# Kernel optimization log

Measured on AMD Instinct MI355X. Metric: run time of the kernel, lower is better.

The kernel has to match this reference:

```python
import jax, jax.numpy as jnp
import numpy as np

B, S, D = 2, 2048, 768
H, STRIDE = 12, 8
HD = D // H  # 64


def setup_inputs() -> dict:
    key = jax.random.key(0)
    k0, k1, k2 = jax.random.split(key, 3)
    x = jax.random.normal(k0, (B, S, D), dtype=jnp.float32)
    qkv_w = jax.random.normal(k1, (3 * D, D), dtype=jnp.float32) * 0.02
    qkv_b = jnp.zeros((3 * D,), dtype=jnp.float32)
    out_w = jax.random.normal(k2, (D, D), dtype=jnp.float32) * 0.02
    out_b = jnp.zeros((D,), dtype=jnp.float32)
    return {"x": x, "qkv_w": qkv_w, "qkv_b": qkv_b, "out_w": out_w, "out_b": out_b}


def _stride_mask(S, stride, causal):
    i = jnp.arange(S)[:, None]
    j = jnp.arange(S)[None, :]
    strided = (j % stride == 0)
    if causal:
        strided = strided & (j <= i)
    # diagonal always attended; previous token attended for i > 0
    return strided | (j == i) | (j == i - 1)


def reference(x, qkv_w, qkv_b, out_w, out_b):
    Bx, Sx, Dx = x.shape
    qkv = x @ qkv_w.T + qkv_b                      # [B,S,3D]
    qkv = qkv.reshape(Bx, Sx, 3, H, HD)
    q, k, v = jnp.transpose(qkv, (2, 0, 3, 1, 4))  # each [B,H,S,HD]
    scale = HD ** -0.5
    attn = jnp.einsum('bhid,bhjd->bhij', q, k) * scale  # [B,H,S,S]
    mask = _stride_mask(Sx, STRIDE, True)          # [S,S] bool
    attn = jnp.where(mask[None, None], attn, -jnp.inf)
    a = jax.nn.softmax(attn, axis=-1)
    # every row has at least the diagonal unmasked, so no NaN rows;
    # nan_to_num kept for exact parity with the torch module
    a = jnp.nan_to_num(a, nan=0.0)
    out = jnp.einsum('bhij,bhjd->bhid', a, v)      # [B,H,S,HD]
    out = jnp.transpose(out, (0, 2, 1, 3)).reshape(Bx, Sx, Dx)
    return out @ out_w.T + out_b
```

## Files before the change

### kernel.cpp

```cpp
#include <hip/hip_runtime.h>
#include <hip/hip_bf16.h>
#include <stdint.h>

#define H_   12
#define S_   2048
#define D_   768
#define HD_  64
#define MS_  256

typedef __bf16 bf16_8 __attribute__((ext_vector_type(8)));
typedef float  f32_4  __attribute__((ext_vector_type(4)));

typedef __attribute__((address_space(1))) void* gas_ptr;
typedef __attribute__((address_space(3))) void* las_ptr;

__device__ __forceinline__ void g2l16(const void* g, void* l) {
  __builtin_amdgcn_global_load_lds((gas_ptr)g, (las_ptr)l, 16, 0, 0);
}

__device__ __forceinline__ f32_4 mfma16(bf16_8 a, bf16_8 b, f32_4 c) {
  return __builtin_amdgcn_mfma_f32_16x16x32_bf16(a, b, c, 0, 0, 0);
}

__device__ __forceinline__ bf16_8 ld8(const __hip_bfloat16* p) {
  return *reinterpret_cast<const bf16_8*>(p);
}

__global__ __launch_bounds__(256) void cvt3_f32_bf16(
    const float* __restrict__ a, const float* __restrict__ b,
    const float* __restrict__ c, __hip_bfloat16* __restrict__ out,
    int na4, int nb4) {
  const int t = blockIdx.x * 256 + threadIdx.x;
  float4 f;
  if (t < na4)            f = reinterpret_cast<const float4*>(a)[t];
  else if (t < na4 + nb4) f = reinterpret_cast<const float4*>(b)[t - na4];
  else                    f = reinterpret_cast<const float4*>(c)[t - na4 - nb4];
  union { __hip_bfloat16 h[4]; ushort4 u; } p;
  p.h[0] = __float2bfloat16(f.x);
  p.h[1] = __float2bfloat16(f.y);
  p.h[2] = __float2bfloat16(f.z);
  p.h[3] = __float2bfloat16(f.w);
  reinterpret_cast<ushort4*>(out)[t] = p.u;
}

template <int MODE, int BN>
__global__ __launch_bounds__(256, 2) void gemm_bt(
    const __hip_bfloat16* __restrict__ A, const __hip_bfloat16* __restrict__ B,
    const float* __restrict__ bias,
    __hip_bfloat16* __restrict__ O0, __hip_bfloat16* __restrict__ O1,
    __hip_bfloat16* __restrict__ O2, __hip_bfloat16* __restrict__ O3,
    __hip_bfloat16* __restrict__ O4, float* __restrict__ OF,
    int M, int N, int K) {
  constexpr int NTJ = BN / 32;
  __shared__ __bf16 sA[128 * 32];
  __shared__ __bf16 sB[BN * 32];
  const int tid  = threadIdx.x;
  const int lane = tid & 63;
  const int wv   = tid >> 6;
  const int m0 = blockIdx.y * 128;
  const int n0 = blockIdx.x * BN;
  const int wr = (wv >> 1) * 64;
  const int wc = (wv & 1) * (BN / 2);

  f32_4 acc[4][NTJ] = {};

  const __hip_bfloat16* aS = A + (size_t)(m0 + (tid >> 2)) * K + ((tid & 3) << 3);
  const __hip_bfloat16* bS = B + (size_t)(n0 + (tid >> 2)) * K + ((tid & 3) << 3);
  const size_t half = (size_t)64 * K;
  __bf16* dA  = &sA[tid * 8];
  __bf16* dA2 = &sA[tid * 8 + 2048];
  __bf16* dB  = &sB[tid * 8];
  __bf16* dB2 = &sB[tid * 8 + 2048];

  const int fr = lane & 15;
  const int kq = (lane >> 4) << 3;

  for (int k0 = 0; k0 < K; k0 += 32) {
    g2l16(aS, dA);
    g2l16(aS + half, dA2);
    g2l16(bS, dB);
    if constexpr (BN == 128) g2l16(bS + half, dB2);
    aS += 32;
    bS += 32;
    __syncthreads();
    bf16_8 af[4], bfm[NTJ];
#pragma unroll
    for (int t = 0; t < 4; ++t)
      af[t] = *reinterpret_cast<const bf16_8*>(&sA[(wr + t * 16 + fr) * 32 + kq]);
#pragma unroll
    for (int t = 0; t < NTJ; ++t)
      bfm[t] = *reinterpret_cast<const bf16_8*>(&sB[(wc + t * 16 + fr) * 32 + kq]);
#pragma unroll
    for (int ti = 0; ti < 4; ++ti)
#pragma unroll
      for (int tj = 0; tj < NTJ; ++tj)
        acc[ti][tj] = mfma16(af[ti], bfm[tj], acc[ti][tj]);
    __syncthreads();
  }

  const int crow = (lane >> 4) << 2;
  const int ccol = lane & 15;
#pragma unroll
  for (int ti = 0; ti < 4; ++ti) {
    const int gmb = m0 + wr + ti * 16 + crow;
#pragma unroll
    for (int tj = 0; tj < NTJ; ++tj) {
      const int gn = n0 + wc + tj * 16 + ccol;
      const float bv = bias[gn];
      if (MODE == 0) {
        const int t   = gn / D_;
        const int rem = gn - t * D_;
        const int hh = rem >> 6, dd = rem & 63;
        __hip_bfloat16* dst = (t == 0) ? O0 : (t == 1) ? O1 : O2;
#pragma unroll
        for (int r = 0; r < 4; ++r) {
          const int gm = gmb + r;
          const int bb = gm >> 11, ss = gm & (S_ - 1);
          const __hip_bfloat16 hv = __float2bfloat16(acc[ti][tj][r] + bv);
          dst[(((size_t)(bb * H_ + hh) << 11) + ss) * HD_ + dd] = hv;
          if (r == 0 && (gmb & 7) == 0) {
            if (t == 1)
              O4[(((size_t)(bb * H_ + hh)) * MS_ + (ss >> 3)) * HD_ + dd] = hv;
            else if (t == 2)
              O3[((size_t)(bb * H_ + hh) * HD_ + dd) * MS_ + (ss >> 3)] = hv;
          }
        }
      } else {
#pragma unroll
        for (int r = 0; r < 4; ++r)
          OF[(size_t)(gmb + r) * D_ + gn] = acc[ti][tj][r] + bv;
      }
    }
  }
}

__global__ __launch_bounds__(256) void attn_mfma(
    const __hip_bfloat16* __restrict__ Q, const __hip_bfloat16* __restrict__ Kb,
    const __hip_bfloat16* __restrict__ Ks, const __hip_bfloat16* __restrict__ Vr,
    const __hip_bfloat16* __restrict__ VsT, __hip_bfloat16* __restrict__ ctx) {
  __shared__ __bf16 pt[4][16 * 40];
  __shared__ float ox[2][64][20];
  const int lane = threadIdx.x & 63;
  const int wv   = threadIdx.x >> 6;
  const int tp   = wv >> 1;
  const int part = wv & 1;
  const int task = blockIdx.x * 2 + tp;
  const int bh   = task >> 7;
  const int i0   = (task & 127) << 4;
  const int lr   = lane & 15;
  const int quad = lane >> 4;
  const float SC = 0.125f * 1.44269504088896340736f;

  const __hip_bfloat16* Kh  = Kb  + ((size_t)bh << 11) * HD_;
  const __hip_bfloat16* Ksh = Ks  + (size_t)bh * MS_ * HD_;
  const __hip_bfloat16* Vrh = Vr  + ((size_t)bh << 11) * HD_;
  const __hip_bfloat16* Vsh = VsT + (size_t)bh * HD_ * MS_;
  __bf16* ptw = pt[wv];

  const int jbase = (i0 >= 8) ? (i0 - 8) : 0;

  bf16_8 vfb[4], kb_[2][2];
  if (part) {
    const __bf16* Vrb = reinterpret_cast<const __bf16*>(Vrh);
#pragma unroll
    for (int ct = 0; ct < 4; ++ct)
#pragma unroll
      for (int e = 0; e < 8; ++e) {
        const int j  = jbase + quad * 8 + e;
        const int jr = (j < S_) ? j : (S_ - 1);
        vfb[ct][e] = Vrb[(size_t)jr * HD_ + ct * 16 + lr];
      }
#pragma unroll
    for (int t = 0; t < 2; ++t) {
      const int j  = jbase + t * 16 + lr;
      const int jr = (j < S_) ? j : (S_ - 1);
      const __hip_bfloat16* kp = Kh + (size_t)jr * HD_ + quad * 8;
      kb_[t][0] = ld8(kp);
      kb_[t][1] = ld8(kp + 32);
    }
  }

  const __hip_bfloat16* qp = Q + (((size_t)bh << 11) + i0 + lr) * HD_ + quad * 8;
  const bf16_8 qf0 = ld8(qp);
  const bf16_8 qf1 = ld8(qp + 32);

  const __bf16 one = (__bf16)1.0f;
  const bf16_8 onesf = {one, one, one, one, one, one, one, one};

  f32_4 Lacc = {}, oacc[4];
#pragma unroll
  for (int ct = 0; ct < 4; ++ct) oacc[ct] = f32_4{0.f, 0.f, 0.f, 0.f};

  const int mmax = (i0 + 15) >> 3;
  const int nstr = (mmax >> 5) + 1;

  auto load_str = [&](int c, bf16_8 (&kf)[2][2], bf16_8 (&vf)[4]) {
    const int mb = c << 5;
#pragma unroll
    for (int t = 0; t < 2; ++t) {
      const __hip_bfloat16* kp = Ksh + (size_t)(mb + t * 16 + lr) * HD_ + quad * 8;
      kf[t][0] = ld8(kp);
      kf[t][1] = ld8(kp + 32);
    }
#pragma unroll
    for (int ct = 0; ct < 4; ++ct)
      vf[ct] = ld8(Vsh + (size_t)(ct * 16 + lr) * MS_ + mb + quad * 8);
  };

  auto softmax_pv = [&](f32_4& s0, f32_4& s1, const bf16_8 (&vf)[4]) {
#pragma unroll
    for (int r = 0; r < 4; ++r) {
      const int row = quad * 4 + r;
      ptw[row * 40 + lr]      = (__bf16)__float2bfloat16(s0[r]);
      ptw[row * 40 + 16 + lr] = (__bf16)__float2bfloat16(s1[r]);
    }
    const bf16_8 pf = *reinterpret_cast<const bf16_8*>(&ptw[lr * 40 + quad * 8]);
#pragma unroll
    for (int ct = 0; ct < 4; ++ct) oacc[ct] = mfma16(pf, vf[ct], oacc[ct]);
    Lacc = mfma16(pf, onesf, Lacc);
  };

  bf16_8 kf[2][2], vf[4], kf2[2][2], vf2[4];
  if (part < nstr) load_str(part, kf, vf);
  for (int c = part; c < nstr; c += 2) {
    const bool more = (c + 2 < nstr);
    if (more) load_str(c + 2, kf2, vf2);
    const int mb = c << 5;

    f32_4 s0 = {}, s1 = {};
    s0 = mfma16(qf0, kf[0][0], s0);
    s0 = mfma16(qf1, kf[0][1], s0);
    s1 = mfma16(qf0, kf[1][0], s1);
    s1 = mfma16(qf1, kf[1][1], s1);

#pragma unroll
    for (int r = 0; r < 4; ++r) {
      const int i = i0 + quad * 4 + r;
      const bool v0 = ((mb + lr) << 3) <= i;
      const bool v1 = ((mb + 16 + lr) << 3) <= i;
      s0[r] = v0 ? exp2f(fminf(s0[r] * SC, 63.f)) : 0.f;
      s1[r] = v1 ? exp2f(fminf(s1[r] * SC, 63.f)) : 0.f;
    }
    softmax_pv(s0, s1, vf);

    if (more) {
#pragma unroll
      for (int t = 0; t < 2; ++t) { kf[t][0] = kf2[t][0]; kf[t][1] = kf2[t][1]; }
#pragma unroll
      for (int ct = 0; ct < 4; ++ct) vf[ct] = vf2[ct];
    }
  }

  if (part) {
    f32_4 s0 = {}, s1 = {};
    s0 = mfma16(qf0, kb_[0][0], s0);
    s0 = mfma16(qf1, kb_[0][1], s0);
    s1 = mfma16(qf0, kb_[1][0], s1);
    s1 = mfma16(qf1, kb_[1][1], s1);

#pragma unroll
    for (int r = 0; r < 4; ++r) {
      const int i = i0 + quad * 4 + r;
      const int j0 = jbase + lr, j1 = jbase + 16 + lr;
      const bool v0 = (j0 == i || j0 == i - 1) && (j0 & 7);
      const bool v1 = (j1 == i || j1 == i - 1) && (j1 & 7);
      s0[r] = v0 ? exp2f(fminf(s0[r] * SC, 63.f)) : 0.f;
      s1[r] = v1 ? exp2f(fminf(s1[r] * SC, 63.f)) : 0.f;
    }
    softmax_pv(s0, s1, vfb);

#pragma unroll
    for (int ct = 0; ct < 4; ++ct)
#pragma unroll
      for (int r = 0; r < 4; ++r) ox[tp][lane][ct * 4 + r] = oacc[ct][r];
#pragma unroll
    for (int r = 0; r < 4; ++r) ox[tp][lane][16 + r] = Lacc[r];
  }
  __syncthreads();

  if (!part) {
#pragma unroll
    for (int ct = 0; ct < 4; ++ct)
#pragma unroll
      for (int r = 0; r < 4; ++r) oacc[ct][r] += ox[tp][lane][ct * 4 + r];
#pragma unroll
    for (int r = 0; r < 4; ++r) Lacc[r] += ox[tp][lane][16 + r];

    const int b = bh / H_;
    const int h = bh - b * H_;
    f32_4 inv;
#pragma unroll
    for (int r = 0; r < 4; ++r) inv[r] = 1.f / Lacc[r];
#pragma unroll
    for (int r = 0; r < 4; ++r) {
      const int i = i0 + quad * 4 + r;
      __hip_bfloat16* cp = ctx + ((size_t)(b * S_ + i)) * D_ + h * HD_ + lr;
#pragma unroll
      for (int ct = 0; ct < 4; ++ct)
        cp[ct * 16] = __float2bfloat16(oacc[ct][r] * inv[r]);
    }
  }
}

extern "C" void kernel_launch(void* const* d_in, const int* in_sizes, int n_in,
                              void* d_out, int out_size, void* d_ws, size_t ws_size,
                              hipStream_t stream) {
  const float* x    = (const float*)d_in[0];
  const float* qkvw = (const float*)d_in[1];
  const float* qkvb = (const float*)d_in[2];
  const float* outw = (const float*)d_in[3];
  const float* outb = (const float*)d_in[4];
  float* out = (float*)d_out;

  const size_t NX  = (size_t)2 * S_ * D_;
  const size_t NW1 = (size_t)3 * D_ * D_;
  const size_t NW2 = (size_t)D_ * D_;
  const size_t NVS = (size_t)2 * H_ * HD_ * MS_;

  __hip_bfloat16* xb  = (__hip_bfloat16*)d_ws;
  __hip_bfloat16* w1b = xb + NX;
  __hip_bfloat16* w2b = w1b + NW1;
  __hip_bfloat16* q   = w2b + NW2;
  __hip_bfloat16* k   = q + NX;
  __hip_bfloat16* vr  = k + NX;
  __hip_bfloat16* vst = vr + NX;
  __hip_bfloat16* ks  = vst + NVS;
  __hip_bfloat16* ctx = ks + NVS;

  const int na4 = (int)(NX / 4), nb4 = (int)(NW1 / 4), nc4 = (int)(NW2 / 4);
  cvt3_f32_bf16<<<dim3((na4 + nb4 + nc4) / 256), 256, 0, stream>>>(
      x, qkvw, outw, xb, na4, nb4);

  gemm_bt<0, 128><<<dim3(2304 / 128, 4096 / 128), 256, 0, stream>>>(
      xb, w1b, qkvb, q, k, vr, vst, ks, nullptr, 4096, 2304, 768);

  attn_mfma<<<dim3(2 * H_ * S_ / 16 / 2), 256, 0, stream>>>(
      q, k, ks, vr, vst, ctx);

  gemm_bt<1, 64><<<dim3(768 / 64, 4096 / 128), 256, 0, stream>>>(
      ctx, w2b, outb, nullptr, nullptr, nullptr, nullptr, nullptr,
      out, 4096, 768, 768);
}
```

Baseline: 148.5 us.

## Compute transposed scores to feed PV MFMA directly from registers, drop LDS staging

Swaps the operand order of the QK^T MFMA so each lane holds a column-major score fragment. That fragment can be used directly as the A operand of 16x16x16 bf16 MFMAs for the PV product and the row-sum, which removes the per-wave LDS write/read round trip that transposed the probabilities. V fragments are split into two 4-wide halves to match. The cost is twice as many (smaller-K) MFMA instructions for PV and the row-sum, and the output accumulator layout must still match the later reduction.

```diff
diff --git a/kernel.cpp b/kernel.cpp
--- a/kernel.cpp
+++ b/kernel.cpp
@@ -9,6 +9,8 @@
 #define MS_  256
 
 typedef __bf16 bf16_8 __attribute__((ext_vector_type(8)));
+typedef __bf16 bf16_4 __attribute__((ext_vector_type(4)));
+typedef short  s16x4  __attribute__((ext_vector_type(4)));
 typedef float  f32_4  __attribute__((ext_vector_type(4)));
 
 typedef __attribute__((address_space(1))) void* gas_ptr;
@@ -22,8 +24,20 @@
   return __builtin_amdgcn_mfma_f32_16x16x32_bf16(a, b, c, 0, 0, 0);
 }
 
+__device__ __forceinline__ f32_4 mfma16k16(bf16_4 a, bf16_4 b, f32_4 c) {
+#if __has_builtin(__builtin_amdgcn_mfma_f32_16x16x16_bf16)
+  return __builtin_amdgcn_mfma_f32_16x16x16_bf16(a, b, c, 0, 0, 0);
+#else
+  return __builtin_amdgcn_mfma_f32_16x16x16bf16_1k(
+      __builtin_bit_cast(s16x4, a), __builtin_bit_cast(s16x4, b), c, 0, 0, 0);
+#endif
+}
+
 __device__ __forceinline__ bf16_8 ld8(const __hip_bfloat16* p) {
   return *reinterpret_cast<const bf16_8*>(p);
+}
+__device__ __forceinline__ bf16_4 ld4(const __hip_bfloat16* p) {
+  return *reinterpret_cast<const bf16_4*>(p);
 }
 
 __global__ __launch_bounds__(256) void cvt3_f32_bf16(
@@ -138,7 +152,6 @@
     const __hip_bfloat16* __restrict__ Q, const __hip_bfloat16* __restrict__ Kb,
     const __hip_bfloat16* __restrict__ Ks, const __hip_bfloat16* __restrict__ Vr,
     const __hip_bfloat16* __restrict__ VsT, __hip_bfloat16* __restrict__ ctx) {
-  __shared__ __bf16 pt[4][16 * 40];
   __shared__ float ox[2][64][20];
   const int lane = threadIdx.x & 63;
   const int wv   = threadIdx.x >> 6;
@@ -155,20 +168,23 @@
   const __hip_bfloat16* Ksh = Ks  + (size_t)bh * MS_ * HD_;
   const __hip_bfloat16* Vrh = Vr  + ((size_t)bh << 11) * HD_;
   const __hip_bfloat16* Vsh = VsT + (size_t)bh * HD_ * MS_;
-  __bf16* ptw = pt[wv];
 
   const int jbase = (i0 >= 8) ? (i0 - 8) : 0;
 
-  bf16_8 vfb[4], kb_[2][2];
+  bf16_4 vfb0[4], vfb1[4];
+  bf16_8 kb_[2][2];
   if (part) {
     const __bf16* Vrb = reinterpret_cast<const __bf16*>(Vrh);
 #pragma unroll
     for (int ct = 0; ct < 4; ++ct)
 #pragma unroll
-      for (int e = 0; e < 8; ++e) {
-        const int j  = jbase + quad * 8 + e;
-        const int jr = (j < S_) ? j : (S_ - 1);
-        vfb[ct][e] = Vrb[(size_t)jr * HD_ + ct * 16 + lr];
+      for (int e = 0; e < 4; ++e) {
+        const int j0 = jbase + quad * 4 + e;
+        const int j1 = j0 + 16;
+        const int jr0 = (j0 < S_) ? j0 : (S_ - 1);
+        const int jr1 = (j1 < S_) ? j1 : (S_ - 1);
+        vfb0[ct][e] = Vrb[(size_t)jr0 * HD_ + ct * 16 + lr];
+        vfb1[ct][e] = Vrb[(size_t)jr1 * HD_ + ct * 16 + lr];
       }
 #pragma unroll
     for (int t = 0; t < 2; ++t) {
@@ -185,7 +201,7 @@
   const bf16_8 qf1 = ld8(qp + 32);
 
   const __bf16 one = (__bf16)1.0f;
-  const bf16_8 onesf = {one, one, one, one, one, one, one, one};
+  const bf16_4 ones4 = {one, one, one, one};
 
   f32_4 Lacc = {}, oacc[4];
 #pragma unroll
@@ -194,7 +210,7 @@
   const int mmax = (i0 + 15) >> 3;
   const int nstr = (mmax >> 5) + 1;
 
-  auto load_str = [&](int c, bf16_8 (&kf)[2][2], bf16_8 (&vf)[4]) {
+  auto load_str = [&](int c, bf16_8 (&kf)[2][2], bf16_4 (&v0)[4], bf16_4 (&v1)[4]) {
     const int mb = c << 5;
 #pragma unroll
     for (int t = 0; t < 2; ++t) {
@@ -203,71 +219,76 @@
       kf[t][1] = ld8(kp + 32);
     }
 #pragma unroll
-    for (int ct = 0; ct < 4; ++ct)
-      vf[ct] = ld8(Vsh + (size_t)(ct * 16 + lr) * MS_ + mb + quad * 8);
+    for (int ct = 0; ct < 4; ++ct) {
+      const __hip_bfloat16* vp = Vsh + (size_t)(ct * 16 + lr) * MS_ + mb + quad * 4;
+      v0[ct] = ld4(vp);
+      v1[ct] = ld4(vp + 16);
+    }
   };
 
-  auto softmax_pv = [&](f32_4& s0, f32_4& s1, const bf16_8 (&vf)[4]) {
-#pragma unroll
-    for (int r = 0; r < 4; ++r) {
-      const int row = quad * 4 + r;
-      ptw[row * 40 + lr]      = (__bf16)__float2bfloat16(s0[r]);
-      ptw[row * 40 + 16 + lr] = (__bf16)__float2bfloat16(s1[r]);
-    }
-    const bf16_8 pf = *reinterpret_cast<const bf16_8*>(&ptw[lr * 40 + quad * 8]);
-#pragma unroll
-    for (int ct = 0; ct < 4; ++ct) oacc[ct] = mfma16(pf, vf[ct], oacc[ct]);
-    Lacc = mfma16(pf, onesf, Lacc);
+  auto pv = [&](const bf16_4& p0, const bf16_4& p1,
+                const bf16_4 (&v0)[4], const bf16_4 (&v1)[4]) {
+#pragma unroll
+    for (int ct = 0; ct < 4; ++ct) {
+      oacc[ct] = mfma16k16(p0, v0[ct], oacc[ct]);
+      oacc[ct] = mfma16k16(p1, v1[ct], oacc[ct]);
+    }
+    Lacc = mfma16k16(p0, ones4, Lacc);
+    Lacc = mfma16k16(p1, ones4, Lacc);
   };
 
-  bf16_8 kf[2][2], vf[4], kf2[2][2], vf2[4];
-  if (part < nstr) load_str(part, kf, vf);
+  bf16_8 kf[2][2], kf2[2][2];
+  bf16_4 vf0[4], vf1[4], vf0b[4], vf1b[4];
+  if (part < nstr) load_str(part, kf, vf0, vf1);
   for (int c = part; c < nstr; c += 2) {
     const bool more = (c + 2 < nstr);
-    if (more) load_str(c + 2, kf2, vf2);
+    if (more) load_str(c + 2, kf2, vf0b, vf1b);
     const int mb = c << 5;
 
-    f32_4 s0 = {}, s1 = {};
-    s0 = mfma16(qf0, kf[0][0], s0);
-    s0 = mfma16(qf1, kf[0][1], s0);
-    s1 = mfma16(qf0, kf[1][0], s1);
-    s1 = mfma16(qf1, kf[1][1], s1);
-
+    f32_4 st0 = {}, st1 = {};
+    st0 = mfma16(kf[0][0], qf0, st0);
+    st0 = mfma16(kf[0][1], qf1, st0);
+    st1 = mfma16(kf[1][0], qf0, st1);
+    st1 = mfma16(kf[1][1], qf1, st1);
+
+    bf16_4 p0, p1;
 #pragma unroll
     for (int r = 0; r < 4; ++r) {
-      const int i = i0 + quad * 4 + r;
-      const bool v0 = ((mb + lr) << 3) <= i;
-      const bool v1 = ((mb + 16 + lr) << 3) <= i;
-      s0[r] = v0 ? exp2f(fminf(s0[r] * SC, 63.f)) : 0.f;
-      s1[r] = v1 ? exp2f(fminf(s1[r] * SC, 63.f)) : 0.f;
-    }
-    softmax_pv(s0, s1, vf);
+      const int i  = i0 + lr;
+      const bool v0 = ((mb + quad * 4 + r) << 3) <= i;
+      const bool v1 = ((mb + 16 + quad * 4 + r) << 3) <= i;
+      p0[r] = (__bf16)__float2bfloat16(v0 ? exp2f(fminf(st0[r] * SC, 63.f)) : 0.f);
+      p1[r] = (__bf16)__float2bfloat16(v1 ? exp2f(fminf(st1[r] * SC, 63.f)) : 0.f);
+    }
+    pv(p0, p1, vf0, vf1);
 
     if (more) {
 #pragma unroll
       for (int t = 0; t < 2; ++t) { kf[t][0] = kf2[t][0]; kf[t][1] = kf2[t][1]; }
 #pragma unroll
-      for (int ct = 0; ct < 4; ++ct) vf[ct] = vf2[ct];
+      for (int ct = 0; ct < 4; ++ct) { vf0[ct] = vf0b[ct]; vf1[ct] = vf1b[ct]; }
     }
   }
 
   if (part) {
-    f32_4 s0 = {}, s1 = {};
-    s0 = mfma16(qf0, kb_[0][0], s0);
-    s0 = mfma16(qf1, kb_[0][1], s0);
-    s1 = mfma16(qf0, kb_[1][0], s1);
-    s1 = mfma16(qf1, kb_[1][1], s1);
-
+    f32_4 st0 = {}, st1 = {};
+    st0 = mfma16(kb_[0][0], qf0, st0);
+    st0 = mfma16(kb_[0][1], qf1, st0);
+    st1 = mfma16(kb_[1][0], qf0, st1);
+    st1 = mfma16(kb_[1][1], qf1, st1);
+
+    bf16_4 p0, p1;
 #pragma unroll
     for (int r = 0; r < 4; ++r) {
-      const int i = i0 + quad * 4 + r;
-      const int j0 = jbase + lr, j1 = jbase + 16 + lr;
+      const int i  = i0 + lr;
+      const int j0 = jbase + quad * 4 + r;
+      const int j1 = j0 + 16;
       const bool v0 = (j0 == i || j0 == i - 1) && (j0 & 7);
       const bool v1 = (j1 == i || j1 == i - 1) && (j1 & 7);
-      s0[r] = v0 ? exp2f(fminf(s0[r] * SC, 63.f)) : 0.f;
-      s1[r] = v1 ? exp2f(fminf(s1[r] * SC, 63.f)) : 0.f;
-    }
-    softmax_pv(s0, s1, vfb);
+      p0[r] = (__bf16)__float2bfloat16(v0 ? exp2f(fminf(st0[r] * SC, 63.f)) : 0.f);
+      p1[r] = (__bf16)__float2bfloat16(v1 ? exp2f(fminf(st1[r] * SC, 63.f)) : 0.f);
+    }
+    pv(p0, p1, vfb0, vfb1);
 
 #pragma unroll
     for (int ct = 0; ct < 4; ++ct)
```

Result: slower. 159.2 us (+7.2%).
